# Kernel optimization log

Hardware: AMD Instinct MI355X
Metric: run time of the kernel (lower is better)

The kernel has to match this reference:

```python
import jax, jax.numpy as jnp
import numpy as np

N = 100000
F_IN = 512
H1 = 256  # nhid*2
H2 = 128  # nhid
C = 4
E = 3200000


def setup_inputs() -> dict:
    key = jax.random.key(0)
    ks = jax.random.split(key, 8)
    x = jax.random.normal(ks[0], (N, F_IN), dtype=jnp.float32)
    edge_index = jax.random.randint(ks[1], (2, E), 0, N, dtype=jnp.int64)
    s = 1.0 / np.sqrt(F_IN)
    W1 = jax.random.uniform(ks[2], (F_IN, H1), jnp.float32, -s, s)
    b1 = jnp.zeros((H1,), jnp.float32)
    s2 = 1.0 / np.sqrt(H1)
    W2 = jax.random.uniform(ks[3], (H1, H2), jnp.float32, -s2, s2)
    b2 = jnp.zeros((H2,), jnp.float32)
    s3 = 1.0 / np.sqrt(H2)
    Wl = jax.random.uniform(ks[4], (H2, C), jnp.float32, -s3, s3)
    bl = jax.random.uniform(ks[5], (C,), jnp.float32, -s3, s3)
    return {"x": x, "edge_index": edge_index, "W1": W1, "b1": b1,
            "W2": W2, "b2": b2, "Wl": Wl, "bl": bl}


def gcn_conv(x, W, b, src, dst, n):
    # PyG GCNConv: add self loops, symmetric normalization D^-1/2 (A+I) D^-1/2
    h = x @ W  # [N, out]
    ones = jnp.ones((src.shape[0],), h.dtype)
    deg = jax.ops.segment_sum(ones, dst, num_segments=n) + 1.0  # +1 self loop
    dinv = jax.lax.rsqrt(deg)
    norm = dinv[src] * dinv[dst]  # [E]
    msg = h[src] * norm[:, None]  # gather + scale
    agg = jax.ops.segment_sum(msg, dst, num_segments=n)  # scatter-add
    agg = agg + h * (dinv * dinv)[:, None]  # self-loop contribution (norm=1/deg)
    return agg + b


def reference(x, edge_index, W1, b1, W2, b2, Wl, bl):
    src, dst = edge_index[0], edge_index[1]
    h = jax.nn.relu(gcn_conv(x, W1, b1, src, dst, N))
    h = jax.nn.relu(gcn_conv(h, W2, b2, src, dst, N))
    logits = h @ Wl + bl
    return jax.nn.log_softmax(logits, axis=-1)
```

## Files before the change

### kernel.cpp

```cpp
#include <hip/hip_runtime.h>
#include <hip/hip_bf16.h>
#include <cstdint>
#include <cstddef>

__device__ __forceinline__ float bf2f(unsigned short u) {
    return __uint_as_float(((unsigned int)u) << 16);
}
__device__ __forceinline__ unsigned short f2bf(float f) {
    unsigned int u = __float_as_uint(f);
    unsigned int r = (u + 0x7fff + ((u >> 16) & 1)) >> 16;
    return (unsigned short)r;
}

using bf16x8 = __attribute__((ext_vector_type(8))) short;
using f32x4  = __attribute__((ext_vector_type(4))) float;
typedef float f32x2 __attribute__((ext_vector_type(2)));

#define FP8_SCALE    64.0f
#define FP8_INVSCALE 0.015625f

__device__ __forceinline__ unsigned char f2fp8(float v) {
    int p = __builtin_amdgcn_cvt_pk_fp8_f32(v, v, 0, false);
    return (unsigned char)(p & 0xFF);
}
__device__ __forceinline__ void acc_fp8x8(unsigned lo, unsigned hi, float* a) {
    f32x2 f0 = __builtin_amdgcn_cvt_pk_f32_fp8((int)lo, false);
    f32x2 f1 = __builtin_amdgcn_cvt_pk_f32_fp8((int)lo, true);
    f32x2 f2 = __builtin_amdgcn_cvt_pk_f32_fp8((int)hi, false);
    f32x2 f3 = __builtin_amdgcn_cvt_pk_f32_fp8((int)hi, true);
    a[0] += f0[0]; a[1] += f0[1]; a[2] += f1[0]; a[3] += f1[1];
    a[4] += f2[0]; a[5] += f2[1]; a[6] += f3[0]; a[7] += f3[1];
}

#define BKT_SHIFT 9
#define BKT_NODES 512
#define BKT_CAP   18432
#define BIN_TILE  4096
#define PAD_G     8
#define BKT_PADMAX (BKT_NODES * (PAD_G - 1))

__global__ __launch_bounds__(256) void bin_kernel(const int* __restrict__ eidx, int E,
                                                  int nb, int ntiles,
                                                  int* __restrict__ gcur,
                                                  unsigned* __restrict__ binned) {
    __shared__ int cnt[256];
    __shared__ int base[256];
    const int tid = threadIdx.x;
    for (int t = blockIdx.x; t < ntiles; t += gridDim.x) {
        cnt[tid] = 0;
        __syncthreads();
        int s[16], d[16];
        unsigned pk[16];
        #pragma unroll
        for (int j = 0; j < 16; ++j) {
            int e = t * BIN_TILE + j * 256 + tid;
            if (e < E) {
                s[j] = eidx[e];
                d[j] = eidx[E + e];
                int b = d[j] >> BKT_SHIFT;
                int r = atomicAdd(&cnt[b], 1);
                pk[j] = ((unsigned)b << 16) | (unsigned)r;
            } else {
                pk[j] = 0xFFFFFFFFu;
            }
        }
        __syncthreads();
        if (tid < nb) {
            int c = cnt[tid];
            base[tid] = c ? atomicAdd(&gcur[tid], c) : 0;
        }
        __syncthreads();
        #pragma unroll
        for (int j = 0; j < 16; ++j) {
            if (pk[j] != 0xFFFFFFFFu) {
                int b = (int)(pk[j] >> 16);
                int pos = base[b] + (int)(pk[j] & 0xFFFFu);
                if (pos < BKT_CAP)
                    binned[(size_t)b * BKT_CAP + pos] =
                        ((unsigned)s[j] << BKT_SHIFT) | ((unsigned)d[j] & (BKT_NODES - 1));
            }
        }
        __syncthreads();
    }
}

__global__ __launch_bounds__(256) void csr_build_kernel(const unsigned* __restrict__ binned,
                                                        const int* __restrict__ gcur,
                                                        int* __restrict__ rowptr,
                                                        int* __restrict__ deg,
                                                        float* __restrict__ dinv,
                                                        int* __restrict__ csr_src,
                                                        int nb, int n) {
    __shared__ int cnt[BKT_NODES];
    __shared__ int sbase[256];
    __shared__ int wsum[4];
    const int b = blockIdx.x;
    const int base_node = b << BKT_SHIFT;
    const int tid = threadIdx.x, lane = tid & 63, wave = tid >> 6;

    int c = (tid < nb) ? (min(gcur[tid], BKT_CAP) + BKT_PADMAX) : 0;
    int inc = c;
    #pragma unroll
    for (int off = 1; off < 64; off <<= 1) {
        int t = __shfl_up(inc, off, 64);
        if (lane >= off) inc += t;
    }
    if (lane == 63) wsum[wave] = inc;
    __syncthreads();
    int wbase = 0;
    #pragma unroll
    for (int w = 0; w < 4; ++w)
        if (w < wave) wbase += wsum[w];
    sbase[tid] = wbase + inc - c;
    __syncthreads();
    const int gb = sbase[b];
    __syncthreads();

    for (int i = tid; i < BKT_NODES; i += 256) cnt[i] = 0;
    __syncthreads();
    const int m = min(gcur[b], BKT_CAP);
    const unsigned* eb = binned + (size_t)b * BKT_CAP;
    for (int i = tid; i < m; i += 256)
        atomicAdd(&cnt[eb[i] & (BKT_NODES - 1)], 1);
    __syncthreads();

    int c0 = cnt[2 * tid], c1 = cnt[2 * tid + 1];
    int pc0 = (c0 + PAD_G - 1) & ~(PAD_G - 1);
    int pc1 = (c1 + PAD_G - 1) & ~(PAD_G - 1);
    int s = pc0 + pc1;
    int inc2 = s;
    #pragma unroll
    for (int off = 1; off < 64; off <<= 1) {
        int t = __shfl_up(inc2, off, 64);
        if (lane >= off) inc2 += t;
    }
    __syncthreads();
    if (lane == 63) wsum[wave] = inc2;
    __syncthreads();
    int wbase2 = 0;
    #pragma unroll
    for (int w = 0; w < 4; ++w)
        if (w < wave) wbase2 += wsum[w];
    int excl = wbase2 + inc2 - s;
    int node0 = base_node + 2 * tid;
    int st0 = gb + excl, st1 = gb + excl + pc0;
    if (node0 < n) {
        rowptr[node0] = st0;
        deg[node0] = pc0;
        dinv[node0] = rsqrtf((float)c0 + 1.0f);
        for (int q = c0; q < pc0; ++q) csr_src[st0 + q] = n;
    }
    if (node0 + 1 < n) {
        rowptr[node0 + 1] = st1;
        deg[node0 + 1] = pc1;
        dinv[node0 + 1] = rsqrtf((float)c1 + 1.0f);
        for (int q = c1; q < pc1; ++q) csr_src[st1 + q] = n;
    }
    __syncthreads();
    cnt[2 * tid] = st0;
    cnt[2 * tid + 1] = st1;
    __syncthreads();

    for (int i = tid; i < m; i += 256) {
        unsigned p = eb[i];
        int pos = atomicAdd(&cnt[p & (BKT_NODES - 1)], 1);
        csr_src[pos] = (int)(p >> BKT_SHIFT);
    }
}

__global__ __launch_bounds__(256) void hist_kernel(const int* __restrict__ dst, int E,
                                                   int* __restrict__ deg) {
    int i = blockIdx.x * blockDim.x + threadIdx.x;
    int stride = gridDim.x * blockDim.x;
    for (int e = i; e < E; e += stride) atomicAdd(&deg[dst[e]], 1);
}

__global__ __launch_bounds__(256) void fill_kernel(const int* __restrict__ eidx, int E,
                                                   int* __restrict__ cursor,
                                                   int* __restrict__ csr_src) {
    int e = blockIdx.x * blockDim.x + threadIdx.x;
    if (e < E) {
        int s = eidx[e];
        int d = eidx[E + e];
        int pos = atomicAdd(&cursor[d], 1);
        csr_src[pos] = s;
    }
}

__global__ __launch_bounds__(256) void scan_kernel(const int* __restrict__ deg,
                                                   int* __restrict__ rowptr, int n) {
    __shared__ int wsum[4];
    __shared__ int carry_s;
    int tid = threadIdx.x, lane = tid & 63, wave = tid >> 6;
    if (tid == 0) carry_s = 0;
    __syncthreads();
    const int CHUNK = 16;
    const int PER_ITER = 256 * CHUNK;
    for (int base = 0; base < n; base += PER_ITER) {
        int idx0 = base + tid * CHUNK;
        int v[CHUNK];
        int s = 0;
        #pragma unroll
        for (int j = 0; j < CHUNK; ++j) {
            int i = idx0 + j;
            v[j] = (i < n) ? deg[i] : 0;
            s += v[j];
        }
        int inc = s;
        #pragma unroll
        for (int off = 1; off < 64; off <<= 1) {
            int t = __shfl_up(inc, off, 64);
            if (lane >= off) inc += t;
        }
        if (lane == 63) wsum[wave] = inc;
        __syncthreads();
        int wbase = 0;
        #pragma unroll
        for (int w = 0; w < 4; ++w)
            if (w < wave) wbase += wsum[w];
        int total_iter = wsum[0] + wsum[1] + wsum[2] + wsum[3];
        int carry = carry_s;
        __syncthreads();
        if (tid == 0) carry_s = carry + total_iter;
        int run = carry + wbase + (inc - s);
        #pragma unroll
        for (int j = 0; j < CHUNK; ++j) {
            int i = idx0 + j;
            if (i < n) rowptr[i] = run;
            run += v[j];
        }
        __syncthreads();
    }
    if (tid == 0) rowptr[n] = carry_s;
}

__global__ __launch_bounds__(256) void dinv_kernel(const int* __restrict__ deg,
                                                   float* __restrict__ dinv, int n) {
    int i = blockIdx.x * blockDim.x + threadIdx.x;
    if (i < n) dinv[i] = rsqrtf((float)deg[i] + 1.0f);
}

__global__ __launch_bounds__(256) void wt_kernel(const float* __restrict__ W1,
                                                 const float* __restrict__ W2,
                                                 unsigned short* __restrict__ W1F,
                                                 unsigned short* __restrict__ W2F) {
    int i = blockIdx.x * 256 + threadIdx.x;
    const int n1 = 512 * 256;
    if (i < n1) {
        int blk = i >> 9, r = i & 511;
        int lane = r >> 3, jj = r & 7;
        int k0 = (blk >> 4) << 5;
        int f = blk & 15;
        int quad = lane >> 4, l16 = lane & 15;
        int k = k0 + quad * 8 + jj;
        int nn = f * 16 + l16;
        W1F[i] = f2bf(W1[(size_t)k * 256 + nn]);
    } else {
        int j = i - n1;
        if (j < 256 * 128) {
            int blk = j >> 9, r = j & 511;
            int lane = r >> 3, jj = r & 7;
            int k0 = (blk >> 3) << 5;
            int f = blk & 7;
            int quad = lane >> 4, l16 = lane & 15;
            int k = k0 + quad * 8 + jj;
            int nn = f * 16 + l16;
            W2F[j] = f2bf(W2[(size_t)k * 128 + nn]);
        }
    }
}

__device__ __forceinline__ bf16x8 load8_as_bf16(const float* p) {
    float4 lo = *reinterpret_cast<const float4*>(p);
    float4 hi = *reinterpret_cast<const float4*>(p + 4);
    bf16x8 r;
    r[0] = (short)f2bf(lo.x); r[1] = (short)f2bf(lo.y);
    r[2] = (short)f2bf(lo.z); r[3] = (short)f2bf(lo.w);
    r[4] = (short)f2bf(hi.x); r[5] = (short)f2bf(hi.y);
    r[6] = (short)f2bf(hi.z); r[7] = (short)f2bf(hi.w);
    return r;
}

__global__ __launch_bounds__(256, 3) void gemm1_kernel(const float* __restrict__ x,
                                                       const unsigned short* __restrict__ W1F,
                                                       const float* __restrict__ dinv,
                                                       unsigned char* __restrict__ C,
                                                       int M) {
    const int tid = threadIdx.x;
    const int wave = tid >> 6, lane = tid & 63;
    const int quad = lane >> 4, l16 = lane & 15;
    const int m0 = blockIdx.x * 64;
    const int arow = m0 + wave * 16 + l16;
    const bool valid = arow < M;
    const float* aptr = x + (size_t)arow * 512 + quad * 8;
    f32x4 acc[4][4] = {};
    for (int k0 = 0; k0 < 512; k0 += 32) {
        bf16x8 af = {};
        if (valid) af = load8_as_bf16(aptr + k0);
        const unsigned short* wp = W1F + (((k0 >> 5) << 4) << 9) + lane * 8;
        #pragma unroll
        for (int i = 0; i < 4; ++i) {
            #pragma unroll
            for (int ct = 0; ct < 4; ++ct) {
                bf16x8 bfr = *reinterpret_cast<const bf16x8*>(wp + (((i << 2) + ct) << 9));
                acc[i][ct] = __builtin_amdgcn_mfma_f32_16x16x32_bf16(af, bfr, acc[i][ct], 0, 0, 0);
            }
        }
    }
    #pragma unroll
    for (int r = 0; r < 4; ++r) {
        int row = m0 + wave * 16 + quad * 4 + r;
        if (row < M) {
            float dv = dinv[row] * FP8_SCALE;
            #pragma unroll
            for (int i = 0; i < 4; ++i)
                #pragma unroll
                for (int ct = 0; ct < 4; ++ct)
                    C[(size_t)row * 256 + i * 64 + ct * 16 + l16] = f2fp8(acc[i][ct][r] * dv);
        }
    }
}

__device__ __forceinline__ int a2_idx(int row, int col) {
    int byte = (row << 9) + (col << 1);
    byte ^= (row & 7) << 4;
    return byte >> 1;
}

__global__ __launch_bounds__(256, 5) void agg1_gemm2_kernel(const unsigned char* __restrict__ hs1,
                                                            const float* __restrict__ dinv,
                                                            const int* __restrict__ rowptr,
                                                            const int* __restrict__ deg,
                                                            const int* __restrict__ csr_src,
                                                            const float* __restrict__ b1,
                                                            const unsigned short* __restrict__ W2F,
                                                            unsigned short* __restrict__ hs2,
                                                            int n) {
    __shared__ __align__(16) short As2[64 * 256];
    const int tid = threadIdx.x;
    const int m0 = blockIdx.x * 64;

    {
        const int lane = tid & 31;
        const int sub = tid >> 5;
        const unsigned char* tab = hs1 + (size_t)lane * 8;
        float4 blo = *(reinterpret_cast<const float4*>(b1) + lane * 2);
        float4 bhi = *(reinterpret_cast<const float4*>(b1) + lane * 2 + 1);
        float bvals[8] = {blo.x, blo.y, blo.z, blo.w, bhi.x, bhi.y, bhi.z, bhi.w};
        for (int g = 0; g < 8; ++g) {
            int row = g * 8 + sub;
            int node = m0 + row;
            float h[8] = {};
            if (node < n) {
                float a[8] = {};
                uint2 v0 = *reinterpret_cast<const uint2*>(tab + (size_t)node * 256);
                acc_fp8x8(v0.x, v0.y, a);
                int e0 = rowptr[node], e1 = e0 + deg[node];
                int p = e0;
                for (; p + 8 <= e1; p += 8) {
                    int s[8];
                    #pragma unroll
                    for (int u = 0; u < 8; ++u) s[u] = csr_src[p + u];
                    uint2 w[8];
                    #pragma unroll
                    for (int u = 0; u < 8; ++u)
                        w[u] = *reinterpret_cast<const uint2*>(tab + (size_t)s[u] * 256);
                    #pragma unroll
                    for (int u = 0; u < 8; ++u)
                        acc_fp8x8(w[u].x, w[u].y, a);
                }
                for (; p < e1; ++p) {
                    int s = csr_src[p];
                    uint2 w = *reinterpret_cast<const uint2*>(tab + (size_t)s * 256);
                    acc_fp8x8(w.x, w.y, a);
                }
                float dv = dinv[node] * FP8_INVSCALE;
                #pragma unroll
                for (int j = 0; j < 8; ++j)
                    h[j] = fmaxf(fmaf(a[j], dv, bvals[j]), 0.f);
            }
            bf16x8 o;
            #pragma unroll
            for (int j = 0; j < 8; ++j) o[j] = (short)f2bf(h[j]);
            *reinterpret_cast<bf16x8*>(&As2[a2_idx(row, lane * 8)]) = o;
        }
    }
    __syncthreads();

    const int wave = tid >> 6, lane = tid & 63;
    const int quad = lane >> 4, l16 = lane & 15;
    const int arow = wave * 16 + l16;
    f32x4 acc[2][4] = {};
    #pragma unroll
    for (int k0 = 0; k0 < 256; k0 += 32) {
        bf16x8 af = *reinterpret_cast<const bf16x8*>(&As2[a2_idx(arow, k0 + quad * 8)]);
        #pragma unroll
        for (int i = 0; i < 2; ++i) {
            #pragma unroll
            for (int ct = 0; ct < 4; ++ct) {
                bf16x8 bfr = *reinterpret_cast<const bf16x8*>(
                    W2F + ((((k0 >> 5) << 3) + i * 4 + ct) << 9) + lane * 8);
                acc[i][ct] = __builtin_amdgcn_mfma_f32_16x16x32_bf16(af, bfr, acc[i][ct], 0, 0, 0);
            }
        }
    }
    #pragma unroll
    for (int r = 0; r < 4; ++r) {
        int row = m0 + wave * 16 + quad * 4 + r;
        if (row < n) {
            float dv = dinv[row];
            #pragma unroll
            for (int i = 0; i < 2; ++i)
                #pragma unroll
                for (int ct = 0; ct < 4; ++ct)
                    hs2[(size_t)row * 128 + i * 64 + ct * 16 + l16] = f2bf(acc[i][ct][r] * dv);
        }
    }
}

__global__ __launch_bounds__(256) void agg2_head_kernel(const unsigned short* __restrict__ hs,
                                                        const float* __restrict__ dinv,
                                                        const int* __restrict__ rowptr,
                                                        const int* __restrict__ deg,
                                                        const int* __restrict__ csr_src,
                                                        const float* __restrict__ bias,
                                                        const float* __restrict__ Wl,
                                                        const float* __restrict__ bl,
                                                        float* __restrict__ out, int n) {
    constexpr int LANES = 16, H = 128, NPB = 16;
    int sub = threadIdx.x / LANES;
    int lane = threadIdx.x % LANES;
    int node = blockIdx.x * NPB + sub;
    if (node >= n) return;
    const unsigned short* tab = hs + (size_t)lane * 8;
    float a[8];
    bf16x8 v0 = *reinterpret_cast<const bf16x8*>(tab + (size_t)node * H);
    #pragma unroll
    for (int j = 0; j < 8; ++j) a[j] = bf2f((unsigned short)v0[j]);
    int e0 = rowptr[node], e1 = e0 + deg[node];
    int p = e0;
    for (; p + 8 <= e1; p += 8) {
        int s[8];
        #pragma unroll
        for (int u = 0; u < 8; ++u) s[u] = csr_src[p + u];
        bf16x8 w[8];
        #pragma unroll
        for (int u = 0; u < 8; ++u)
            w[u] = *reinterpret_cast<const bf16x8*>(tab + (size_t)s[u] * H);
        #pragma unroll
        for (int u = 0; u < 8; ++u)
            #pragma unroll
            for (int j = 0; j < 8; ++j) a[j] += bf2f((unsigned short)w[u][j]);
    }
    for (; p < e1; ++p) {
        int s = csr_src[p];
        bf16x8 w = *reinterpret_cast<const bf16x8*>(tab + (size_t)s * H);
        #pragma unroll
        for (int j = 0; j < 8; ++j) a[j] += bf2f((unsigned short)w[j]);
    }
    float dv = dinv[node];
    float4 blo = *(reinterpret_cast<const float4*>(bias) + lane * 2);
    float4 bhi = *(reinterpret_cast<const float4*>(bias) + lane * 2 + 1);
    float bvals[8] = {blo.x, blo.y, blo.z, blo.w, bhi.x, bhi.y, bhi.z, bhi.w};
    float h[8];
    #pragma unroll
    for (int j = 0; j < 8; ++j)
        h[j] = fmaxf(fmaf(a[j], dv, bvals[j]), 0.f);
    float p0 = 0.f, p1 = 0.f, p2 = 0.f, p3 = 0.f;
    #pragma unroll
    for (int j = 0; j < 8; ++j) {
        float4 w = *reinterpret_cast<const float4*>(Wl + (size_t)(lane * 8 + j) * 4);
        p0 = fmaf(h[j], w.x, p0); p1 = fmaf(h[j], w.y, p1);
        p2 = fmaf(h[j], w.z, p2); p3 = fmaf(h[j], w.w, p3);
    }
    #pragma unroll
    for (int m = 1; m < 16; m <<= 1) {
        p0 += __shfl_xor(p0, m, 16);
        p1 += __shfl_xor(p1, m, 16);
        p2 += __shfl_xor(p2, m, 16);
        p3 += __shfl_xor(p3, m, 16);
    }
    if (lane == 0) {
        p0 += bl[0]; p1 += bl[1]; p2 += bl[2]; p3 += bl[3];
        float mx = fmaxf(fmaxf(p0, p1), fmaxf(p2, p3));
        float s = __expf(p0 - mx) + __expf(p1 - mx) + __expf(p2 - mx) + __expf(p3 - mx);
        float lse = mx + __logf(s);
        *(reinterpret_cast<float4*>(out) + node) = make_float4(p0 - lse, p1 - lse, p2 - lse, p3 - lse);
    }
}

extern "C" void kernel_launch(void* const* d_in, const int* in_sizes, int n_in,
                              void* d_out, int out_size, void* d_ws, size_t ws_size,
                              hipStream_t stream) {
    const float* x  = (const float*)d_in[0];
    const int* eidx = (const int*)d_in[1];
    const float* W1 = (const float*)d_in[2];
    const float* b1 = (const float*)d_in[3];
    const float* W2 = (const float*)d_in[4];
    const float* b2 = (const float*)d_in[5];
    const float* Wl = (const float*)d_in[6];
    const float* bl = (const float*)d_in[7];
    float* out = (float*)d_out;

    const int n = in_sizes[0] / 512;
    const int E = in_sizes[1] / 2;
    const int nb = (n + BKT_NODES - 1) >> BKT_SHIFT;

    char* ws = (char*)d_ws;
    size_t off = 0;
    auto alloc = [&](size_t bytes) -> void* {
        void* p = ws + off;
        off += (bytes + 255) & ~(size_t)255;
        return p;
    };
    unsigned char*  hA  = (unsigned char*)alloc((size_t)(n + 1) * 256);
    unsigned short* hB  = (unsigned short*)alloc((size_t)(n + 1) * 128 * 2);
    unsigned short* W1F = (unsigned short*)alloc((size_t)256 * 512 * 2);
    unsigned short* W2F = (unsigned short*)alloc((size_t)128 * 256 * 2);
    int* deg     = (int*)alloc((size_t)n * 4);
    int* rowptr  = (int*)alloc(((size_t)n + 1) * 4);
    int* cursor  = (int*)alloc((size_t)n * 4);
    float* dinv  = (float*)alloc((size_t)n * 4);
    int* csr_src = (int*)alloc(((size_t)E + (size_t)nb * BKT_PADMAX + 64) * 4);
    int* gcur    = (int*)alloc((size_t)nb * 4);
    size_t need_binned = off + (size_t)nb * BKT_CAP * 4 + 256;
    unsigned* binned = (unsigned*)alloc((size_t)nb * BKT_CAP * 4);

    if (need_binned <= ws_size && nb <= 256 && n < (1 << 23)) {
        hipMemsetAsync(gcur, 0, (size_t)nb * 4, stream);
        int ntiles = (E + BIN_TILE - 1) / BIN_TILE;
        bin_kernel<<<dim3(256), dim3(256), 0, stream>>>(eidx, E, nb, ntiles, gcur, binned);
        csr_build_kernel<<<dim3(nb), dim3(256), 0, stream>>>(binned, gcur, rowptr, deg, dinv,
                                                             csr_src, nb, n);
    } else {
        hipMemsetAsync(deg, 0, (size_t)n * 4, stream);
        hist_kernel<<<dim3(1024), dim3(256), 0, stream>>>(eidx + E, E, deg);
        scan_kernel<<<dim3(1), dim3(256), 0, stream>>>(deg, rowptr, n);
        dinv_kernel<<<dim3((n + 255) / 256), dim3(256), 0, stream>>>(deg, dinv, n);
        hipMemcpyAsync(cursor, rowptr, (size_t)n * 4, hipMemcpyDeviceToDevice, stream);
        fill_kernel<<<dim3((E + 255) / 256), dim3(256), 0, stream>>>(eidx, E, cursor, csr_src);
    }

    hipMemsetAsync(hA + (size_t)n * 256, 0, 256, stream);
    hipMemsetAsync(hB + (size_t)n * 128, 0, 128 * 2, stream);

    wt_kernel<<<dim3((512 * 256 + 256 * 128 + 255) / 256), dim3(256), 0, stream>>>(
        W1, W2, W1F, W2F);

    const int mblocks = (n + 63) / 64;

    gemm1_kernel<<<dim3(mblocks), dim3(256), 0, stream>>>(x, W1F, dinv, hA, n);

    agg1_gemm2_kernel<<<dim3(mblocks), dim3(256), 0, stream>>>(
        hA, dinv, rowptr, deg, csr_src, b1, W2F, hB, n);

    agg2_head_kernel<<<dim3((n + 15) / 16), dim3(256), 0, stream>>>(
        hB, dinv, rowptr, deg, csr_src, b2, Wl, bl, out, n);
}
```

Baseline: 712.1 us.

## Stage gemm1 A tiles through LDS with async double-buffered global_load_lds

The first GEMM now loads x tiles into double-buffered shared memory with swizzled async global-to-LDS loads, prefetching the next K-chunk while MFMAs run on the current one. The float-to-bf16 conversion switches to packed hardware v_cvt_pk_bf16_f32 instructions instead of manual rounding, and the occupancy hint rises from 3 to 4 blocks. This is meant to hide the latency of streaming the large fp32 input. It costs 32KB of LDS per block and a barrier per K step.

After: 694.3 us. 2.5% less time.

```diff
diff --git a/kernel.cpp b/kernel.cpp
--- a/kernel.cpp
+++ b/kernel.cpp
@@ -30,6 +30,15 @@
     f32x2 f3 = __builtin_amdgcn_cvt_pk_f32_fp8((int)hi, true);
     a[0] += f0[0]; a[1] += f0[1]; a[2] += f1[0]; a[3] += f1[1];
     a[4] += f2[0]; a[5] += f2[1]; a[6] += f3[0]; a[7] += f3[1];
+}
+
+__device__ __forceinline__ bf16x8 cvt8(float4 a, float4 b) {
+    union { unsigned u[4]; bf16x8 v; } r;
+    asm("v_cvt_pk_bf16_f32 %0, %1, %2" : "=v"(r.u[0]) : "v"(a.x), "v"(a.y));
+    asm("v_cvt_pk_bf16_f32 %0, %1, %2" : "=v"(r.u[1]) : "v"(a.z), "v"(a.w));
+    asm("v_cvt_pk_bf16_f32 %0, %1, %2" : "=v"(r.u[2]) : "v"(b.x), "v"(b.y));
+    asm("v_cvt_pk_bf16_f32 %0, %1, %2" : "=v"(r.u[3]) : "v"(b.z), "v"(b.w));
+    return r.v;
 }
 
 #define BKT_SHIFT 9
@@ -270,53 +279,73 @@
     }
 }
 
-__device__ __forceinline__ bf16x8 load8_as_bf16(const float* p) {
-    float4 lo = *reinterpret_cast<const float4*>(p);
-    float4 hi = *reinterpret_cast<const float4*>(p + 4);
-    bf16x8 r;
-    r[0] = (short)f2bf(lo.x); r[1] = (short)f2bf(lo.y);
-    r[2] = (short)f2bf(lo.z); r[3] = (short)f2bf(lo.w);
-    r[4] = (short)f2bf(hi.x); r[5] = (short)f2bf(hi.y);
-    r[6] = (short)f2bf(hi.z); r[7] = (short)f2bf(hi.w);
-    return r;
-}
-
-__global__ __launch_bounds__(256, 3) void gemm1_kernel(const float* __restrict__ x,
+__global__ __launch_bounds__(256, 4) void gemm1_kernel(const float* __restrict__ x,
                                                        const unsigned short* __restrict__ W1F,
                                                        const float* __restrict__ dinv,
                                                        unsigned char* __restrict__ C,
                                                        int M) {
+    __shared__ float As[2][4096];
     const int tid = threadIdx.x;
     const int wave = tid >> 6, lane = tid & 63;
     const int quad = lane >> 4, l16 = lane & 15;
     const int m0 = blockIdx.x * 64;
-    const int arow = m0 + wave * 16 + l16;
-    const bool valid = arow < M;
-    const float* aptr = x + (size_t)arow * 512 + quad * 8;
+
+    const float* sbase[4];
+    #pragma unroll
+    for (int c = 0; c < 4; ++c) {
+        int row  = (wave * 4 + c) * 4 + (lane >> 4);
+        int grow = min(m0 + row, M - 1);
+        int scb  = ((lane & 15) << 4) ^ ((row & 7) << 4);
+        sbase[c] = x + (size_t)grow * 512 + (scb >> 2);
+    }
+    const int r   = wave * 16 + l16;
+    const int swz = (r & 7) << 4;
+    const int rb  = r * 256;
+
+    #pragma unroll
+    for (int c = 0; c < 4; ++c)
+        __builtin_amdgcn_global_load_lds(sbase[c], &As[0][(wave * 4 + c) * 256], 16, 0, 0);
+    __syncthreads();
+
     f32x4 acc[4][4] = {};
-    for (int k0 = 0; k0 < 512; k0 += 32) {
-        bf16x8 af = {};
-        if (valid) af = load8_as_bf16(aptr + k0);
-        const unsigned short* wp = W1F + (((k0 >> 5) << 4) << 9) + lane * 8;
-        #pragma unroll
-        for (int i = 0; i < 4; ++i) {
-            #pragma unroll
-            for (int ct = 0; ct < 4; ++ct) {
-                bf16x8 bfr = *reinterpret_cast<const bf16x8*>(wp + (((i << 2) + ct) << 9));
-                acc[i][ct] = __builtin_amdgcn_mfma_f32_16x16x32_bf16(af, bfr, acc[i][ct], 0, 0, 0);
+    for (int t = 0; t < 8; ++t) {
+        const int cur = t & 1;
+        if (t < 7) {
+            #pragma unroll
+            for (int c = 0; c < 4; ++c)
+                __builtin_amdgcn_global_load_lds(sbase[c] + (t + 1) * 64,
+                                                 &As[cur ^ 1][(wave * 4 + c) * 256], 16, 0, 0);
+        }
+        const char* ab = reinterpret_cast<const char*>(&As[cur][0]);
+        #pragma unroll
+        for (int ks = 0; ks < 2; ++ks) {
+            int cb = (ks << 7) + (quad << 5);
+            float4 a0 = *reinterpret_cast<const float4*>(ab + rb + (cb ^ swz));
+            float4 a1 = *reinterpret_cast<const float4*>(ab + rb + ((cb + 16) ^ swz));
+            bf16x8 af = cvt8(a0, a1);
+            const unsigned short* wp = W1F + ((((t << 1) + ks) << 4) << 9) + lane * 8;
+            #pragma unroll
+            for (int i = 0; i < 4; ++i) {
+                #pragma unroll
+                for (int ct = 0; ct < 4; ++ct) {
+                    bf16x8 bfr = *reinterpret_cast<const bf16x8*>(wp + (((i << 2) + ct) << 9));
+                    acc[i][ct] = __builtin_amdgcn_mfma_f32_16x16x32_bf16(af, bfr, acc[i][ct], 0, 0, 0);
+                }
             }
         }
-    }
-    #pragma unroll
-    for (int r = 0; r < 4; ++r) {
-        int row = m0 + wave * 16 + quad * 4 + r;
+        __syncthreads();
+    }
+
+    #pragma unroll
+    for (int rr = 0; rr < 4; ++rr) {
+        int row = m0 + wave * 16 + quad * 4 + rr;
         if (row < M) {
             float dv = dinv[row] * FP8_SCALE;
             #pragma unroll
             for (int i = 0; i < 4; ++i)
                 #pragma unroll
                 for (int ct = 0; ct < 4; ++ct)
-                    C[(size_t)row * 256 + i * 64 + ct * 16 + l16] = f2fp8(acc[i][ct][r] * dv);
+                    C[(size_t)row * 256 + i * 64 + ct * 16 + l16] = f2fp8(acc[i][ct][rr] * dv);
         }
     }
 }
```
